# Kernel optimization log

Measured on AMD Instinct MI355X. Metric: run time of the kernel, lower is better.

The kernel has to match this reference:

```python
import jax, jax.numpy as jnp
import numpy as np

B, S, D = 64, 4096, 256

def setup_inputs() -> dict:
    key = jax.random.key(0)
    k1, k2, k3 = jax.random.split(key, 3)
    x = jax.random.normal(k1, (B, S, D), dtype=jnp.float32)
    # glorot-scale params
    W = jax.random.normal(k2, (D, D), dtype=jnp.float32) * (1.0 / np.sqrt(D))
    b = jnp.zeros((D,), dtype=jnp.float32)
    u = jax.random.normal(k3, (D, 1), dtype=jnp.float32) * (1.0 / np.sqrt(D))
    return {"x": x, "W": W, "b": b, "u": u}

def reference(x, W, b, u):
    # uit: [B,S,D] = tanh(x @ W + b)
    uit = jnp.tanh(jnp.einsum('bsd,de->bse', x, W) + b)
    # score: [B,S]
    score = jnp.einsum('bsd,d->bs', uit, u[:, 0])
    weights = jax.nn.softmax(score, axis=1)          # [B,S]
    context = jnp.einsum('bs,bsd->bd', weights, x)   # [B,D]
    return (context, weights)
```

## Files before the change

kernel.cpp:

```cpp
#include <hip/hip_runtime.h>
#include <hip/hip_bf16.h>
#include <cstdint>
#include <cstddef>

#define B_ 64
#define S_ 4096
#define D_ 256
#define BM 64
#define BK 32
#define NBLK (B_ * S_ / BM)
#define BLKS_PER_B (S_ / BM)

typedef __attribute__((ext_vector_type(8))) short short8;
typedef __attribute__((ext_vector_type(4))) float f32x4;
typedef __attribute__((ext_vector_type(4))) float f4;

__device__ __forceinline__ short f2bf(float f) {
  union { float f; uint32_t u; } v; v.f = f;
  uint32_t r = v.u + 0x7FFFu + ((v.u >> 16) & 1u);
  return (short)(r >> 16);
}

__device__ __forceinline__ short f2bf_i(float f) {
  union { __hip_bfloat16 b; short s; } v;
  v.b = __float2bfloat16(f);
  return v.s;
}

__device__ __forceinline__ float fast_tanh(float z) {
  return 1.0f - 2.0f * __builtin_amdgcn_rcpf(__expf(2.0f * z) + 1.0f);
}

__device__ __forceinline__ void gload_lds16(const short* g, short* l) {
  __builtin_amdgcn_global_load_lds(
      (const __attribute__((address_space(1))) int*)(g),
      (__attribute__((address_space(3))) int*)(l), 16, 0, 0);
}

__global__ void k_pack(const float* __restrict__ W, short* __restrict__ wt) {
  int idx = blockIdx.x * 1024 + threadIdx.x;
  int n = idx & 255, k = idx >> 8;
  int out = (k >> 5) * 8192 +
            (((n >> 4) * 64 + ((k >> 3) & 3) * 16 + (n & 15)) << 3) + (k & 7);
  wt[out] = f2bf(W[k * 256 + n]);
}

#define WAITV(N) asm volatile("s_waitcnt vmcnt(" #N ")" ::: "memory")
#define FENCE()  asm volatile("" ::: "memory")

#define STAGE(BUF, KC)                                                        \
  {                                                                           \
    _Pragma("unroll")                                                         \
    for (int i_ = 0; i_ < 4; ++i_) {                                          \
      int c_ = i_ * 256 + tid;                                                \
      gload_lds16(wt + (KC) * 8192 + c_ * 8, &lsB[BUF][c_ * 8]);              \
    }                                                                         \
  }

#define ITER(KC, VM, SCA, SCB, SLA, SLB, DOSTAGE, DOLOAD)                     \
  {                                                                           \
    if (DOSTAGE) STAGE(((KC) + 1) & 1, (KC) + 1);                             \
    if (DOLOAD) {                                                             \
      SLA = *(const f4*)(xrow + ((KC) + 2) * 32);                             \
      SLB = *(const f4*)(xrow + ((KC) + 2) * 32 + 4);                         \
    }                                                                         \
    WAITV(VM);                                                                \
    asm volatile("s_waitcnt lgkmcnt(0)" ::: "memory");                        \
    __builtin_amdgcn_sched_barrier(0);                                        \
    __builtin_amdgcn_s_barrier();                                             \
    FENCE();                                                                  \
    short8 fr_;                                                               \
    fr_[0]=f2bf_i(SCA[0]); fr_[1]=f2bf_i(SCA[1]); fr_[2]=f2bf_i(SCA[2]); fr_[3]=f2bf_i(SCA[3]); \
    fr_[4]=f2bf_i(SCB[0]); fr_[5]=f2bf_i(SCB[1]); fr_[6]=f2bf_i(SCB[2]); fr_[7]=f2bf_i(SCB[3]); \
    _Pragma("unroll")                                                         \
    for (int nf_ = 0; nf_ < 16; ++nf_) {                                      \
      short8 bfr_ = *(const short8*)&lsB[(KC) & 1][nf_ * 512 + boff];         \
      acc[nf_] = __builtin_amdgcn_mfma_f32_16x16x32_bf16(fr_, bfr_, acc[nf_], 0, 0, 0); \
    }                                                                         \
    FENCE();                                                                  \
    __builtin_amdgcn_s_barrier();                                             \
    FENCE();                                                                  \
  }

__global__ __launch_bounds__(256, 3)
void k_scores(const float* __restrict__ x, const short* __restrict__ wt,
              const float* __restrict__ bias, const float* __restrict__ u,
              float* __restrict__ ws_scores, float* __restrict__ ws_m,
              float* __restrict__ ws_l, float* __restrict__ ws_c) {
  __shared__ __align__(16) short lsB[2][D_ * BK];
  __shared__ __align__(8) float bu[D_ * 2];
  __shared__ float score_lds[BM];
  __shared__ float e_lds[BM];
  __shared__ float red_lds[1];

  const int tid  = threadIdx.x;
  const int bid  = blockIdx.x;
  const int m0   = bid * BM;
  const int lane = tid & 63;
  const int wv   = tid >> 6;
  const int cl   = lane & 15;
  const int gr   = lane >> 4;
  const int boff = lane * 8;

  bu[tid * 2]     = bias[tid];
  bu[tid * 2 + 1] = u[tid];

  f32x4 acc[16];
#pragma unroll
  for (int j = 0; j < 16; ++j) acc[j] = (f32x4){0.f, 0.f, 0.f, 0.f};

  const float* xrow = x + (size_t)(m0 + wv * 16 + cl) * D_ + gr * 8;

  f4 s0a, s0b, s1a, s1b, s2a, s2b;
  s0a = *(const f4*)(xrow);       s0b = *(const f4*)(xrow + 4);
  STAGE(0, 0);
  s1a = *(const f4*)(xrow + 32);  s1b = *(const f4*)(xrow + 36);

  ITER(0, 8, s0a, s0b, s2a, s2b, 1, 1)
  ITER(1, 8, s1a, s1b, s0a, s0b, 1, 1)
  ITER(2, 8, s2a, s2b, s1a, s1b, 1, 1)
  ITER(3, 8, s0a, s0b, s2a, s2b, 1, 1)
  ITER(4, 8, s1a, s1b, s0a, s0b, 1, 1)
  ITER(5, 8, s2a, s2b, s1a, s1b, 1, 1)
  ITER(6, 6, s0a, s0b, s0a, s0b, 1, 0)
  ITER(7, 0, s1a, s1b, s0a, s0b, 0, 0)

  float p0 = 0.f, p1 = 0.f, p2 = 0.f, p3 = 0.f;
#pragma unroll
  for (int nf = 0; nf < 16; ++nf) {
    float bb = bu[(nf * 16 + cl) * 2];
    float uu = bu[(nf * 16 + cl) * 2 + 1];
    p0 += fast_tanh(acc[nf][0] + bb) * uu;
    p1 += fast_tanh(acc[nf][1] + bb) * uu;
    p2 += fast_tanh(acc[nf][2] + bb) * uu;
    p3 += fast_tanh(acc[nf][3] + bb) * uu;
  }
#pragma unroll
  for (int m = 1; m < 16; m <<= 1) {
    p0 += __shfl_xor(p0, m);
    p1 += __shfl_xor(p1, m);
    p2 += __shfl_xor(p2, m);
    p3 += __shfl_xor(p3, m);
  }
  if (cl == 0) {
    int r = wv * 16 + gr * 4;
    score_lds[r + 0] = p0;
    score_lds[r + 1] = p1;
    score_lds[r + 2] = p2;
    score_lds[r + 3] = p3;
    ws_scores[m0 + r + 0] = p0;
    ws_scores[m0 + r + 1] = p1;
    ws_scores[m0 + r + 2] = p2;
    ws_scores[m0 + r + 3] = p3;
  }
  __syncthreads();
  if (tid < 64) {
    float v = score_lds[tid];
#pragma unroll
    for (int m = 32; m >= 1; m >>= 1) v = fmaxf(v, __shfl_xor(v, m));
    if (tid == 0) red_lds[0] = v;
  }
  __syncthreads();
  float mb = red_lds[0];
  if (tid < BM) e_lds[tid] = __expf(score_lds[tid] - mb);
  __syncthreads();
  if (tid < 64) {
    float v = e_lds[tid];
#pragma unroll
    for (int m = 32; m >= 1; m >>= 1) v += __shfl_xor(v, m);
    if (tid == 0) { ws_m[bid] = mb; ws_l[bid] = v; }
  }
  float cacc = 0.f;
  const float* xp = x + (size_t)m0 * D_ + tid;
#pragma unroll 4
  for (int s = 0; s < BM; ++s) cacc = fmaf(e_lds[s], xp[(size_t)s * D_], cacc);
  ws_c[bid * D_ + tid] = cacc;
}

__global__ __launch_bounds__(1024)
void k_epi(const float* __restrict__ ws_m, const float* __restrict__ ws_l,
           const float* __restrict__ ws_c, const float* __restrict__ ws_scores,
           float* __restrict__ out_ctx, float* __restrict__ out_w) {
  __shared__ float fac[BLKS_PER_B];
  __shared__ float MLs[2];
  const int b = blockIdx.x, tid = threadIdx.x;

  if (tid < 64) {
    float m = ws_m[b * BLKS_PER_B + tid];
    float l = ws_l[b * BLKS_PER_B + tid];
    float M = m;
#pragma unroll
    for (int o = 32; o >= 1; o >>= 1) M = fmaxf(M, __shfl_xor(M, o));
    float f = __expf(m - M);
    fac[tid] = f;
    float L = l * f;
#pragma unroll
    for (int o = 32; o >= 1; o >>= 1) L += __shfl_xor(L, o);
    if (tid == 0) { MLs[0] = M; MLs[1] = L; }
  }
  __syncthreads();
  const float M = MLs[0], L = MLs[1];
  const float invL = 1.0f / L;

  if (tid < D_) {
    float c = 0.f;
#pragma unroll 8
    for (int i = 0; i < BLKS_PER_B; ++i)
      c = fmaf(fac[i], ws_c[(size_t)(b * BLKS_PER_B + i) * D_ + tid], c);
    out_ctx[b * D_ + tid] = c * invL;
  }
#pragma unroll
  for (int r = 0; r < 4; ++r) {
    int s = r * 1024 + tid;
    out_w[b * S_ + s] = __expf(ws_scores[b * S_ + s] - M) * invL;
  }
}

extern "C" void kernel_launch(void* const* d_in, const int* in_sizes, int n_in,
                              void* d_out, int out_size, void* d_ws, size_t ws_size,
                              hipStream_t stream) {
  (void)in_sizes; (void)n_in; (void)out_size; (void)ws_size;
  const float* x    = (const float*)d_in[0];
  const float* W    = (const float*)d_in[1];
  const float* bias = (const float*)d_in[2];
  const float* u    = (const float*)d_in[3];
  float* out_ctx = (float*)d_out;
  float* out_w   = (float*)d_out + B_ * D_;

  char* ws = (char*)d_ws;
  short* wt        = (short*)(ws + 0);
  float* ws_scores = (float*)(ws + 131072);
  float* ws_m      = (float*)(ws + 1179648);
  float* ws_l      = (float*)(ws + 1196032);
  float* ws_c      = (float*)(ws + 1212416);

  hipLaunchKernelGGL(k_pack, dim3(64), dim3(1024), 0, stream, W, wt);
  hipLaunchKernelGGL(k_scores, dim3(NBLK), dim3(256), 0, stream,
                     x, wt, bias, u, ws_scores, ws_m, ws_l, ws_c);
  hipLaunchKernelGGL(k_epi, dim3(B_), dim3(1024), 0, stream,
                     ws_m, ws_l, ws_c, ws_scores, out_ctx, out_w);
}
```

Before: 112.3 us.

## Switch score GEMM to 32x32x16 MFMA with 2x2 wave tiling

Replaces the 16x16x32 bf16 MFMA with 32x32x16 MFMA and retiles the block so each wave computes a 32-row by 128-column quadrant instead of 16 rows by all 256 columns. W is repacked to match the new B-fragment layout, and x prefetch registers double to feed two K-halves per chunk. Each wave now reads half as much W from LDS and issues fewer, larger MFMAs. The cost is a cross-wave partial-score merge through LDS. The softmax max, exp and sum steps are also folded into one pass to drop a barrier.

```diff
diff --git a/kernel.cpp b/kernel.cpp
--- a/kernel.cpp
+++ b/kernel.cpp
@@ -12,7 +12,7 @@
 #define BLKS_PER_B (S_ / BM)
 
 typedef __attribute__((ext_vector_type(8))) short short8;
-typedef __attribute__((ext_vector_type(4))) float f32x4;
+typedef __attribute__((ext_vector_type(16))) float f32x16;
 typedef __attribute__((ext_vector_type(4))) float f4;
 
 __device__ __forceinline__ short f2bf(float f) {
@@ -39,10 +39,11 @@
 
 __global__ void k_pack(const float* __restrict__ W, short* __restrict__ wt) {
   int idx = blockIdx.x * 1024 + threadIdx.x;
-  int n = idx & 255, k = idx >> 8;
-  int out = (k >> 5) * 8192 +
-            (((n >> 4) * 64 + ((k >> 3) & 3) * 16 + (n & 15)) << 3) + (k & 7);
-  wt[out] = f2bf(W[k * 256 + n]);
+  int j = idx & 7, l = (idx >> 3) & 63, ct = (idx >> 9) & 7;
+  int sp = (idx >> 12) & 1, kc = idx >> 13;
+  int k = kc * 32 + sp * 16 + ((l >> 5) << 3) + j;
+  int n = ct * 32 + (l & 31);
+  wt[idx] = f2bf(W[k * 256 + n]);
 }
 
 #define WAITV(N) asm volatile("s_waitcnt vmcnt(" #N ")" ::: "memory")
@@ -57,25 +58,34 @@
     }                                                                         \
   }
 
-#define ITER(KC, VM, SCA, SCB, SLA, SLB, DOSTAGE, DOLOAD)                     \
+#define ITER(KC, VM, CA0, CA1, CA2, CA3, LA0, LA1, LA2, LA3, DOSTAGE, DOLOAD) \
   {                                                                           \
     if (DOSTAGE) STAGE(((KC) + 1) & 1, (KC) + 1);                             \
     if (DOLOAD) {                                                             \
-      SLA = *(const f4*)(xrow + ((KC) + 2) * 32);                             \
-      SLB = *(const f4*)(xrow + ((KC) + 2) * 32 + 4);                         \
+      LA0 = *(const f4*)(xrow + ((KC) + 2) * 32);                             \
+      LA1 = *(const f4*)(xrow + ((KC) + 2) * 32 + 4);                         \
+      LA2 = *(const f4*)(xrow + ((KC) + 2) * 32 + 16);                        \
+      LA3 = *(const f4*)(xrow + ((KC) + 2) * 32 + 20);                        \
     }                                                                         \
     WAITV(VM);                                                                \
     asm volatile("s_waitcnt lgkmcnt(0)" ::: "memory");                        \
     __builtin_amdgcn_sched_barrier(0);                                        \
     __builtin_amdgcn_s_barrier();                                             \
     FENCE();                                                                  \
-    short8 fr_;                                                               \
-    fr_[0]=f2bf_i(SCA[0]); fr_[1]=f2bf_i(SCA[1]); fr_[2]=f2bf_i(SCA[2]); fr_[3]=f2bf_i(SCA[3]); \
-    fr_[4]=f2bf_i(SCB[0]); fr_[5]=f2bf_i(SCB[1]); fr_[6]=f2bf_i(SCB[2]); fr_[7]=f2bf_i(SCB[3]); \
+    short8 f0_, f1_;                                                          \
+    f0_[0]=f2bf_i(CA0[0]); f0_[1]=f2bf_i(CA0[1]); f0_[2]=f2bf_i(CA0[2]); f0_[3]=f2bf_i(CA0[3]); \
+    f0_[4]=f2bf_i(CA1[0]); f0_[5]=f2bf_i(CA1[1]); f0_[6]=f2bf_i(CA1[2]); f0_[7]=f2bf_i(CA1[3]); \
+    f1_[0]=f2bf_i(CA2[0]); f1_[1]=f2bf_i(CA2[1]); f1_[2]=f2bf_i(CA2[2]); f1_[3]=f2bf_i(CA2[3]); \
+    f1_[4]=f2bf_i(CA3[0]); f1_[5]=f2bf_i(CA3[1]); f1_[6]=f2bf_i(CA3[2]); f1_[7]=f2bf_i(CA3[3]); \
     _Pragma("unroll")                                                         \
-    for (int nf_ = 0; nf_ < 16; ++nf_) {                                      \
-      short8 bfr_ = *(const short8*)&lsB[(KC) & 1][nf_ * 512 + boff];         \
-      acc[nf_] = __builtin_amdgcn_mfma_f32_16x16x32_bf16(fr_, bfr_, acc[nf_], 0, 0, 0); \
+    for (int ct_ = 0; ct_ < 4; ++ct_) {                                       \
+      short8 b_ = *(const short8*)&lsB[(KC) & 1][(ctbase + ct_) * 512 + boff];\
+      acc[ct_] = __builtin_amdgcn_mfma_f32_32x32x16_bf16(f0_, b_, acc[ct_], 0, 0, 0); \
+    }                                                                         \
+    _Pragma("unroll")                                                         \
+    for (int ct_ = 0; ct_ < 4; ++ct_) {                                       \
+      short8 b_ = *(const short8*)&lsB[(KC) & 1][4096 + (ctbase + ct_) * 512 + boff]; \
+      acc[ct_] = __builtin_amdgcn_mfma_f32_32x32x16_bf16(f1_, b_, acc[ct_], 0, 0, 0); \
     }                                                                         \
     FENCE();                                                                  \
     __builtin_amdgcn_s_barrier();                                             \
@@ -89,87 +99,84 @@
               float* __restrict__ ws_l, float* __restrict__ ws_c) {
   __shared__ __align__(16) short lsB[2][D_ * BK];
   __shared__ __align__(8) float bu[D_ * 2];
-  __shared__ float score_lds[BM];
+  __shared__ float score_part[BM][2];
   __shared__ float e_lds[BM];
-  __shared__ float red_lds[1];
 
   const int tid  = threadIdx.x;
   const int bid  = blockIdx.x;
   const int m0   = bid * BM;
   const int lane = tid & 63;
   const int wv   = tid >> 6;
-  const int cl   = lane & 15;
-  const int gr   = lane >> 4;
-  const int boff = lane * 8;
+  const int rg32 = (wv & 1) * 32;
+  const int cgi  = wv >> 1;
+  const int l31  = lane & 31;
+  const int hi   = lane >> 5;
+  const int ctbase = cgi * 4;
+  const int boff   = lane * 8;
 
   bu[tid * 2]     = bias[tid];
   bu[tid * 2 + 1] = u[tid];
 
-  f32x4 acc[16];
-#pragma unroll
-  for (int j = 0; j < 16; ++j) acc[j] = (f32x4){0.f, 0.f, 0.f, 0.f};
-
-  const float* xrow = x + (size_t)(m0 + wv * 16 + cl) * D_ + gr * 8;
-
-  f4 s0a, s0b, s1a, s1b, s2a, s2b;
-  s0a = *(const f4*)(xrow);       s0b = *(const f4*)(xrow + 4);
+  f32x16 acc[4];
+#pragma unroll
+  for (int t = 0; t < 4; ++t)
+#pragma unroll
+    for (int i = 0; i < 16; ++i) acc[t][i] = 0.f;
+
+  const float* xrow = x + (size_t)(m0 + rg32 + l31) * D_ + hi * 8;
+
+  f4 ga0, ga1, ga2, ga3, gb0, gb1, gb2, gb3, gc0, gc1, gc2, gc3;
+  ga0 = *(const f4*)(xrow);       ga1 = *(const f4*)(xrow + 4);
+  ga2 = *(const f4*)(xrow + 16);  ga3 = *(const f4*)(xrow + 20);
   STAGE(0, 0);
-  s1a = *(const f4*)(xrow + 32);  s1b = *(const f4*)(xrow + 36);
-
-  ITER(0, 8, s0a, s0b, s2a, s2b, 1, 1)
-  ITER(1, 8, s1a, s1b, s0a, s0b, 1, 1)
-  ITER(2, 8, s2a, s2b, s1a, s1b, 1, 1)
-  ITER(3, 8, s0a, s0b, s2a, s2b, 1, 1)
-  ITER(4, 8, s1a, s1b, s0a, s0b, 1, 1)
-  ITER(5, 8, s2a, s2b, s1a, s1b, 1, 1)
-  ITER(6, 6, s0a, s0b, s0a, s0b, 1, 0)
-  ITER(7, 0, s1a, s1b, s0a, s0b, 0, 0)
-
-  float p0 = 0.f, p1 = 0.f, p2 = 0.f, p3 = 0.f;
-#pragma unroll
-  for (int nf = 0; nf < 16; ++nf) {
-    float bb = bu[(nf * 16 + cl) * 2];
-    float uu = bu[(nf * 16 + cl) * 2 + 1];
-    p0 += fast_tanh(acc[nf][0] + bb) * uu;
-    p1 += fast_tanh(acc[nf][1] + bb) * uu;
-    p2 += fast_tanh(acc[nf][2] + bb) * uu;
-    p3 += fast_tanh(acc[nf][3] + bb) * uu;
-  }
-#pragma unroll
-  for (int m = 1; m < 16; m <<= 1) {
-    p0 += __shfl_xor(p0, m);
-    p1 += __shfl_xor(p1, m);
-    p2 += __shfl_xor(p2, m);
-    p3 += __shfl_xor(p3, m);
-  }
-  if (cl == 0) {
-    int r = wv * 16 + gr * 4;
-    score_lds[r + 0] = p0;
-    score_lds[r + 1] = p1;
-    score_lds[r + 2] = p2;
-    score_lds[r + 3] = p3;
-    ws_scores[m0 + r + 0] = p0;
-    ws_scores[m0 + r + 1] = p1;
-    ws_scores[m0 + r + 2] = p2;
-    ws_scores[m0 + r + 3] = p3;
+  gb0 = *(const f4*)(xrow + 32);  gb1 = *(const f4*)(xrow + 36);
+  gb2 = *(const f4*)(xrow + 48);  gb3 = *(const f4*)(xrow + 52);
+
+  ITER(0, 12, ga0, ga1, ga2, ga3, gc0, gc1, gc2, gc3, 1, 1)
+  ITER(1, 12, gb0, gb1, gb2, gb3, ga0, ga1, ga2, ga3, 1, 1)
+  ITER(2, 12, gc0, gc1, gc2, gc3, gb0, gb1, gb2, gb3, 1, 1)
+  ITER(3, 12, ga0, ga1, ga2, ga3, gc0, gc1, gc2, gc3, 1, 1)
+  ITER(4, 12, gb0, gb1, gb2, gb3, ga0, ga1, ga2, ga3, 1, 1)
+  ITER(5, 12, gc0, gc1, gc2, gc3, gb0, gb1, gb2, gb3, 1, 1)
+  ITER(6, 8,  ga0, ga1, ga2, ga3, ga0, ga1, ga2, ga3, 1, 0)
+  ITER(7, 0,  gb0, gb1, gb2, gb3, ga0, ga1, ga2, ga3, 0, 0)
+
+  float bbv[4], uuv[4];
+#pragma unroll
+  for (int ct = 0; ct < 4; ++ct) {
+    int col = cgi * 128 + ct * 32 + l31;
+    bbv[ct] = bu[col * 2];
+    uuv[ct] = bu[col * 2 + 1];
+  }
+#pragma unroll
+  for (int i = 0; i < 16; ++i) {
+    float v = 0.f;
+#pragma unroll
+    for (int ct = 0; ct < 4; ++ct)
+      v += fast_tanh(acc[ct][i] + bbv[ct]) * uuv[ct];
+#pragma unroll
+    for (int m = 1; m < 32; m <<= 1) v += __shfl_xor(v, m);
+    if (l31 == 0) {
+      int r = rg32 + (i & 3) + 8 * (i >> 2) + 4 * hi;
+      score_part[r][cgi] = v;
+    }
   }
   __syncthreads();
+
   if (tid < 64) {
-    float v = score_lds[tid];
-#pragma unroll
-    for (int m = 32; m >= 1; m >>= 1) v = fmaxf(v, __shfl_xor(v, m));
-    if (tid == 0) red_lds[0] = v;
+    float s = score_part[tid][0] + score_part[tid][1];
+    ws_scores[m0 + tid] = s;
+    float mx = s;
+#pragma unroll
+    for (int m = 1; m < 64; m <<= 1) mx = fmaxf(mx, __shfl_xor(mx, m));
+    float e = __expf(s - mx);
+    e_lds[tid] = e;
+    float l = e;
+#pragma unroll
+    for (int m = 1; m < 64; m <<= 1) l += __shfl_xor(l, m);
+    if (tid == 0) { ws_m[bid] = mx; ws_l[bid] = l; }
   }
   __syncthreads();
-  float mb = red_lds[0];
-  if (tid < BM) e_lds[tid] = __expf(score_lds[tid] - mb);
-  __syncthreads();
-  if (tid < 64) {
-    float v = e_lds[tid];
-#pragma unroll
-    for (int m = 32; m >= 1; m >>= 1) v += __shfl_xor(v, m);
-    if (tid == 0) { ws_m[bid] = mb; ws_l[bid] = v; }
-  }
   float cacc = 0.f;
   const float* xp = x + (size_t)m0 * D_ + tid;
 #pragma unroll 4
```

New measurement: 127.4 us. +13.4%, slower.
